# Kernel optimization log

Measured on AMD Instinct MI355X. Metric: run time of the kernel, lower is better.

## Reference

```python
import jax, jax.numpy as jnp
import numpy as np

N_NODES = 50000
N_EDGES = 600000
N_REL = 8
D_IN = 128
D_OUT = 128


def setup_inputs() -> dict:
    key = jax.random.key(0)
    ks = jax.random.split(key, 12)
    s = 1.0 / np.sqrt(D_IN)
    s2 = 1.0 / np.sqrt(2 * D_IN)
    return {
        "x": jax.random.normal(ks[0], (N_NODES, D_IN), jnp.float32),
        "src": jax.random.randint(ks[1], (N_EDGES,), 0, N_NODES, jnp.int32),
        "dst": jax.random.randint(ks[2], (N_EDGES,), 0, N_NODES, jnp.int32),
        "etype": jax.random.randint(ks[3], (N_EDGES,), 0, N_REL, jnp.int32),
        "Wrel": jax.random.normal(ks[4], (N_REL, D_IN, D_OUT), jnp.float32) * s,
        "Wloop": jax.random.normal(ks[5], (D_IN, D_OUT), jnp.float32) * s,
        "brel": jax.random.normal(ks[6], (D_OUT,), jnp.float32) * s,
        "W1": jax.random.normal(ks[7], (2 * D_IN, 2 * D_IN), jnp.float32) * s2,
        "b1": jax.random.normal(ks[8], (2 * D_IN,), jnp.float32) * s2,
        "W2": jax.random.normal(ks[9], (2 * D_IN, D_OUT), jnp.float32) * s2,
        "b2": jax.random.normal(ks[10], (D_OUT,), jnp.float32) * s2,
    }


def rel_graph_conv(x, src, dst, etype, Wrel, Wloop, brel):
    # low_mem style: transform node features once per relation, then gather per edge.
    xW = jnp.einsum('ni,rio->rno', x, Wrel)          # [R, N, D_OUT]
    msg = xW[etype, src]                              # [E, D_OUT] gather by (rel, src)
    agg = jax.ops.segment_sum(msg, dst, num_segments=N_NODES)  # scatter-add to dst
    return agg + x @ Wloop + brel                     # self-loop + bias (DGL defaults)


def reference(x, src, dst, etype, Wrel, Wloop, brel, W1, b1, W2, b2):
    mid = rel_graph_conv(x, src, dst, etype, Wrel, Wloop, brel)
    h = jnp.concatenate([x, mid], axis=1)             # [N, 2*D_IN]
    h = jax.nn.relu(h @ W1 + b1)
    return h @ W2 + b2
```

## Files before the change

### kernel.cpp

```cpp
#include <hip/hip_runtime.h>

#define N_NODES 50000
#define N_EDGES 600000
#define N_REL 8
#define NT_PAD 50176
#define N_TILES 196

typedef __attribute__((ext_vector_type(8))) short bf16x8;
typedef __attribute__((ext_vector_type(4))) float f32x4;

__device__ __forceinline__ ushort f2b(float f) {
    union { float f; unsigned u; } v; v.f = f;
    unsigned r = v.u + 0x7FFFu + ((v.u >> 16) & 1u);
    return (ushort)(r >> 16);
}
__device__ __forceinline__ float b2f(ushort s) {
    union { unsigned u; float f; } v; v.u = ((unsigned)s) << 16;
    return v.f;
}
__device__ __forceinline__ float asf(unsigned u) {
    union { unsigned u; float f; } v; v.u = u;
    return v.f;
}


__global__ void conv_f32_bf16(const float* __restrict__ in, ushort* __restrict__ outb) {
    int i = (blockIdx.x * 256 + threadIdx.x) * 4;
    float4 f = *(const float4*)(in + i);
    ushort4 o; o.x = f2b(f.x); o.y = f2b(f.y); o.z = f2b(f.z); o.w = f2b(f.w);
    *(ushort4*)(outb + i) = o;
}

__global__ void transpose_wts3(const float* __restrict__ Wloop, const float* __restrict__ Wrel,
                               const float* __restrict__ W1, const float* __restrict__ W2,
                               ushort* __restrict__ wt) {
    int y = blockIdx.y;
    if (y == 0) {
        for (int idx = blockIdx.x * 256 + threadIdx.x; idx < 128 * 1152; idx += gridDim.x * 256) {
            int c = idx / 1152, kg = idx - c * 1152;
            float v = (kg < 1024) ? Wrel[(size_t)((kg >> 7) * 128 + (kg & 127)) * 128 + c]
                                  : Wloop[(size_t)(kg - 1024) * 128 + c];
            wt[idx] = f2b(v);
        }
    } else if (y == 1) {
        for (int idx = blockIdx.x * 256 + threadIdx.x; idx < 256 * 256; idx += gridDim.x * 256) {
            int c = idx >> 8, k = idx & 255;
            wt[147456 + idx] = f2b(W1[k * 256 + c]);
        }
    } else {
        for (int idx = blockIdx.x * 256 + threadIdx.x; idx < 128 * 256; idx += gridDim.x * 256) {
            int c = idx >> 8, k = idx & 255;
            wt[212992 + idx] = f2b(W2[k * 128 + c]);
        }
    }
}

template<int NPH, int KMODE, int AS, int CTOT, int OMODE>
__global__ __launch_bounds__(256, 2) void mfma_gemm(
        const ushort* __restrict__ A0, const ushort* __restrict__ A1,
        const ushort* __restrict__ Bt, const float* __restrict__ bias,
        void* __restrict__ outv) {
    __shared__ ushort bs[2][128 * 136];
    const int t = threadIdx.x;
    const int wave = t >> 6, lane = t & 63;
    const int lr = lane & 15, lg = lane >> 4;
    const int wr = (wave >> 1) * 64, wc = (wave & 1) * 64;
    const int row0 = blockIdx.x * 128;
    const ushort* Btb = Bt + (size_t)blockIdx.y * 128 * (NPH * 128);
    const int sgk = (t & 15) * 8;
    const int sc0 = t >> 4;

#define STAGE_LOAD(p)                                                              \
    _Pragma("unroll")                                                              \
    for (int it = 0; it < 8; ++it)                                                 \
        sreg[it] = *(const bf16x8*)(Btb + (size_t)(sc0 + it * 16) * (NPH * 128) +  \
                                    (p) * 128 + sgk);

#define STAGE_WRITE(b)                                                             \
    _Pragma("unroll")                                                              \
    for (int it = 0; it < 8; ++it)                                                 \
        *(bf16x8*)(&bs[b][(sc0 + it * 16) * 136 + sgk]) = sreg[it];

#define LOAD_AF(p, dstf)                                                           \
    {                                                                              \
        const ushort* Ap; int as_;                                                 \
        if (KMODE == 0) {                                                          \
            if ((p) < 8) { Ap = A0 + (p) * 128; as_ = 1024; }                      \
            else         { Ap = A1;             as_ = 128;  }                      \
        } else { Ap = (p) ? A1 : A0; as_ = AS; }                                   \
        _Pragma("unroll")                                                          \
        for (int rt = 0; rt < 4; ++rt) {                                           \
            int ar = row0 + wr + rt * 16 + lr;                                     \
            if (ar >= N_NODES) ar = 0;                                             \
            _Pragma("unroll")                                                      \
            for (int kc = 0; kc < 4; ++kc)                                         \
                dstf[rt][kc] = *(const bf16x8*)(Ap + (size_t)ar * as_ + kc * 32 + lg * 8); \
        }                                                                          \
    }

    f32x4 acc[4][4];
#pragma unroll
    for (int rt = 0; rt < 4; ++rt)
#pragma unroll
        for (int nt = 0; nt < 4; ++nt) acc[rt][nt] = (f32x4){0.f, 0.f, 0.f, 0.f};

    bf16x8 af[4][4], afn[4][4], sreg[8];

    STAGE_LOAD(0);
    LOAD_AF(0, af);
    STAGE_WRITE(0);
    __syncthreads();

#pragma unroll
    for (int p = 0; p < NPH; ++p) {
        if (p + 1 < NPH) {
            STAGE_LOAD(p + 1);
            LOAD_AF(p + 1, afn);
        }
        const ushort* bcur = bs[p & 1];
#pragma unroll
        for (int kc = 0; kc < 4; ++kc) {
            bf16x8 bf[4];
#pragma unroll
            for (int nt = 0; nt < 4; ++nt)
                bf[nt] = *(const bf16x8*)(bcur + (wc + nt * 16 + lr) * 136 + kc * 32 + lg * 8);
#pragma unroll
            for (int rt = 0; rt < 4; ++rt)
#pragma unroll
                for (int nt = 0; nt < 4; ++nt)
                    acc[rt][nt] = __builtin_amdgcn_mfma_f32_16x16x32_bf16(af[rt][kc], bf[nt], acc[rt][nt], 0, 0, 0);
        }
        if (p + 1 < NPH) {
            STAGE_WRITE((p + 1) & 1);
        }
        __syncthreads();
        if (p + 1 < NPH) {
#pragma unroll
            for (int rt = 0; rt < 4; ++rt)
#pragma unroll
                for (int kc = 0; kc < 4; ++kc) af[rt][kc] = afn[rt][kc];
        }
    }

    const int colbase = blockIdx.y * 128;
#pragma unroll
    for (int rt = 0; rt < 4; ++rt) {
#pragma unroll
        for (int nt = 0; nt < 4; ++nt) {
            const int col = colbase + wc + nt * 16 + lr;
            const float bv = bias[col];
#pragma unroll
            for (int j = 0; j < 4; ++j) {
                const int r = row0 + wr + rt * 16 + lg * 4 + j;
                if (r >= N_NODES) continue;
                float vv = acc[rt][nt][j] + bv;
                if (OMODE == 0) {
                    ((float*)outv)[(size_t)r * CTOT + col] = vv;
                } else if (OMODE == 2) {
                    ((ushort*)outv)[(size_t)r * CTOT + col] = f2b(fmaxf(vv, 0.f));
                } else {
                    ((ushort*)outv)[(size_t)r * 128 + col] = f2b(vv);
                }
            }
        }
    }
#undef STAGE_LOAD
#undef STAGE_WRITE
#undef LOAD_AF
}


__global__ void zero_cnt(int* __restrict__ cnt) {
    int i = blockIdx.x * 256 + threadIdx.x;
    if (i < NT_PAD) cnt[i] = 0;
}

__global__ void hist_dst(const int* __restrict__ dst, int* __restrict__ cnt) {
    int e = blockIdx.x * 256 + threadIdx.x;
    if (e < N_EDGES) atomicAdd(&cnt[dst[e]], 1);
}

__global__ void scan_tiles(const int* __restrict__ cnt, int* __restrict__ tincl, int* __restrict__ bsum) {
    __shared__ int s[256];
    int i = blockIdx.x * 256 + threadIdx.x;
    int v = cnt[i];
    s[threadIdx.x] = v;
    __syncthreads();
    for (int off = 1; off < 256; off <<= 1) {
        int add = (threadIdx.x >= off) ? s[threadIdx.x - off] : 0;
        __syncthreads();
        s[threadIdx.x] += add;
        __syncthreads();
    }
    tincl[i] = s[threadIdx.x];
    if (threadIdx.x == 255) bsum[blockIdx.x] = s[255];
}

__global__ void scan_bsum(const int* __restrict__ bsum, int* __restrict__ bex) {
    __shared__ int s[256];
    int v = (threadIdx.x < N_TILES) ? bsum[threadIdx.x] : 0;
    s[threadIdx.x] = v;
    __syncthreads();
    for (int off = 1; off < 256; off <<= 1) {
        int add = (threadIdx.x >= off) ? s[threadIdx.x - off] : 0;
        __syncthreads();
        s[threadIdx.x] += add;
        __syncthreads();
    }
    if (threadIdx.x < N_TILES) bex[threadIdx.x] = s[threadIdx.x] - v;
}

__global__ void finalize_base(const int* __restrict__ cnt, const int* __restrict__ tincl,
                              const int* __restrict__ bex, int* __restrict__ base,
                              int* __restrict__ cursor) {
    int i = blockIdx.x * 256 + threadIdx.x;
    int b = tincl[i] - cnt[i] + bex[blockIdx.x];
    base[i] = b; cursor[i] = b;
}

__global__ void scatter_ids(const int* __restrict__ src, const int* __restrict__ dst,
                            const int* __restrict__ et, int* __restrict__ cursor,
                            unsigned* __restrict__ sorted) {
    int e = blockIdx.x * 256 + threadIdx.x;
    if (e >= N_EDGES) return;
    int pos = atomicAdd(&cursor[dst[e]], 1);
    sorted[pos] = ((unsigned)src[e] << 3) | (unsigned)et[e];
}


#define ACC_ADD(sd, v)                                                       \
    {                                                                        \
        float lo = asf((v) << 16);                                           \
        float hi = asf((v) & 0xffff0000u);                                   \
        switch ((sd) & 7u) {                                                 \
            case 0: a0[0] += lo; a1[0] += hi; asm volatile(""); break;       \
            case 1: a0[1] += lo; a1[1] += hi; asm volatile(""); break;       \
            case 2: a0[2] += lo; a1[2] += hi; asm volatile(""); break;       \
            case 3: a0[3] += lo; a1[3] += hi; asm volatile(""); break;       \
            case 4: a0[4] += lo; a1[4] += hi; asm volatile(""); break;       \
            case 5: a0[5] += lo; a1[5] += hi; asm volatile(""); break;       \
            case 6: a0[6] += lo; a1[6] += hi; asm volatile(""); break;       \
            default: a0[7] += lo; a1[7] += hi; asm volatile(""); break;      \
        }                                                                    \
    }

__global__ __launch_bounds__(256) void gather_agg(
        const unsigned* __restrict__ sorted, const int* __restrict__ base,
        const int* __restrict__ cnt, const ushort* __restrict__ xbf,
        ushort* __restrict__ agg) {
    const int w = threadIdx.x >> 6, lane = threadIdx.x & 63;
    const int n = blockIdx.x * 4 + w;
    const int b = base[n], c = cnt[n];
    const int loff = lane * 2;

    float a0[8], a1[8];
#pragma unroll
    for (int r = 0; r < 8; ++r) { a0[r] = 0.f; a1[r] = 0.f; }

    const unsigned* sp = sorted + b;
    int i = 0;
    for (; i + 4 <= c; i += 4) {
        unsigned s0 = __builtin_amdgcn_readfirstlane(sp[i]);
        unsigned s1 = __builtin_amdgcn_readfirstlane(sp[i + 1]);
        unsigned s2 = __builtin_amdgcn_readfirstlane(sp[i + 2]);
        unsigned s3 = __builtin_amdgcn_readfirstlane(sp[i + 3]);
        unsigned v0 = *(const unsigned*)(xbf + ((size_t)(s0 >> 3) << 7) + loff);
        unsigned v1 = *(const unsigned*)(xbf + ((size_t)(s1 >> 3) << 7) + loff);
        unsigned v2 = *(const unsigned*)(xbf + ((size_t)(s2 >> 3) << 7) + loff);
        unsigned v3 = *(const unsigned*)(xbf + ((size_t)(s3 >> 3) << 7) + loff);
        ACC_ADD(s0, v0); ACC_ADD(s1, v1); ACC_ADD(s2, v2); ACC_ADD(s3, v3);
    }
    for (; i < c; ++i) {
        unsigned sd = __builtin_amdgcn_readfirstlane(sp[i]);
        unsigned v = *(const unsigned*)(xbf + ((size_t)(sd >> 3) << 7) + loff);
        ACC_ADD(sd, v);
    }
#pragma unroll
    for (int r = 0; r < 8; ++r) {
        unsigned pk = (unsigned)f2b(a0[r]) | ((unsigned)f2b(a1[r]) << 16);
        *(unsigned*)(agg + (size_t)n * 1024 + r * 128 + loff) = pk;
    }
}
#undef ACC_ADD


extern "C" void kernel_launch(void* const* d_in, const int* in_sizes, int n_in,
                              void* d_out, int out_size, void* d_ws, size_t ws_size,
                              hipStream_t stream) {
    const float* x     = (const float*)d_in[0];
    const int*   src   = (const int*)  d_in[1];
    const int*   dst   = (const int*)  d_in[2];
    const int*   etype = (const int*)  d_in[3];
    const float* Wrel  = (const float*)d_in[4];
    const float* Wloop = (const float*)d_in[5];
    const float* brel  = (const float*)d_in[6];
    const float* W1    = (const float*)d_in[7];
    const float* b1    = (const float*)d_in[8];
    const float* W2    = (const float*)d_in[9];
    const float* b2    = (const float*)d_in[10];
    float* out = (float*)d_out;

    char* ws = (char*)d_ws;
    ushort* agg   = (ushort*)ws;
    ushort* wt    = (ushort*)(ws + 102400000);
    char* meta    = ws + 102891520;
    int* cnt      = (int*)(meta);
    int* base     = (int*)(meta + 200704);
    int* cursor   = (int*)(meta + 401408);
    int* tincl    = (int*)(meta + 602112);
    int* bsum     = (int*)(meta + 802816);
    int* bex      = (int*)(meta + 803840);
    unsigned* sorted = (unsigned*)(meta + 804864);
    ushort* xbf   = (ushort*)(ws + 106096384);
    ushort* midbf = (ushort*)(ws + 118896384);

    const ushort* wst = wt;
    const ushort* w1t = wt + 147456;
    const ushort* w2t = wt + 212992;
    ushort* h = agg;

    conv_f32_bf16<<<6250, 256, 0, stream>>>(x, xbf);
    transpose_wts3<<<dim3(64, 3), 256, 0, stream>>>(Wloop, Wrel, W1, W2, wt);

    zero_cnt<<<N_TILES, 256, 0, stream>>>(cnt);
    hist_dst<<<(N_EDGES + 255) / 256, 256, 0, stream>>>(dst, cnt);
    scan_tiles<<<N_TILES, 256, 0, stream>>>(cnt, tincl, bsum);
    scan_bsum<<<1, 256, 0, stream>>>(bsum, bex);
    finalize_base<<<N_TILES, 256, 0, stream>>>(cnt, tincl, bex, base, cursor);
    scatter_ids<<<(N_EDGES + 255) / 256, 256, 0, stream>>>(src, dst, etype, cursor, sorted);

    gather_agg<<<N_NODES / 4, 256, 0, stream>>>(sorted, base, cnt, xbf, agg);

    mfma_gemm<9, 0, 0, 128, 4><<<dim3(391, 1), 256, 0, stream>>>(agg, xbf, wst, brel, (void*)midbf);

    mfma_gemm<2, 1, 128, 256, 2><<<dim3(391, 2), 256, 0, stream>>>(xbf, midbf, w1t, b1, (void*)h);

    mfma_gemm<2, 1, 256, 128, 0><<<dim3(391, 1), 256, 0, stream>>>(h, h + 128, w2t, b2, out);
}
```

Measured before the change: 222.7 us.

## Halve GEMM tile rows and K-step to raise occupancy across all three GEMMs

Each MFMA GEMM block now covers 64 rows instead of 128 and steps K in chunks of 64 instead of 128. This halves LDS use and register footprint, allowing launch bounds of 4 blocks per CU and doubling the grid to 782 blocks. The register double-buffering of A fragments is dropped, so A loads are issued synchronously each phase. The change trades prefetch overlap and per-block reuse of the B tile for more waves in flight to hide latency, with more barriers and phases per block.

```diff
diff --git a/kernel.cpp b/kernel.cpp
--- a/kernel.cpp
+++ b/kernel.cpp
@@ -56,95 +56,88 @@
 }
 
 template<int NPH, int KMODE, int AS, int CTOT, int OMODE>
-__global__ __launch_bounds__(256, 2) void mfma_gemm(
+__global__ __launch_bounds__(256, 4) void mfma_gemm(
         const ushort* __restrict__ A0, const ushort* __restrict__ A1,
         const ushort* __restrict__ Bt, const float* __restrict__ bias,
         void* __restrict__ outv) {
-    __shared__ ushort bs[2][128 * 136];
+    __shared__ ushort bs[2][128 * 72];
     const int t = threadIdx.x;
     const int wave = t >> 6, lane = t & 63;
     const int lr = lane & 15, lg = lane >> 4;
-    const int wr = (wave >> 1) * 64, wc = (wave & 1) * 64;
-    const int row0 = blockIdx.x * 128;
-    const ushort* Btb = Bt + (size_t)blockIdx.y * 128 * (NPH * 128);
-    const int sgk = (t & 15) * 8;
-    const int sc0 = t >> 4;
+    const int wr = (wave >> 1) * 32, wc = (wave & 1) * 64;
+    const int row0 = blockIdx.x * 64;
+    const int KTOT = NPH * 64;
+    const ushort* Btb = Bt + (size_t)blockIdx.y * 128 * KTOT;
+    const int sgk = (t & 7) * 8;
+    const int sc0 = t >> 3;
 
 #define STAGE_LOAD(p)                                                              \
     _Pragma("unroll")                                                              \
-    for (int it = 0; it < 8; ++it)                                                 \
-        sreg[it] = *(const bf16x8*)(Btb + (size_t)(sc0 + it * 16) * (NPH * 128) +  \
-                                    (p) * 128 + sgk);
+    for (int it = 0; it < 4; ++it)                                                 \
+        sreg[it] = *(const bf16x8*)(Btb + (size_t)(sc0 + it * 32) * KTOT +         \
+                                    (p) * 64 + sgk);
 
 #define STAGE_WRITE(b)                                                             \
     _Pragma("unroll")                                                              \
-    for (int it = 0; it < 8; ++it)                                                 \
-        *(bf16x8*)(&bs[b][(sc0 + it * 16) * 136 + sgk]) = sreg[it];
-
-#define LOAD_AF(p, dstf)                                                           \
+    for (int it = 0; it < 4; ++it)                                                 \
+        *(bf16x8*)(&bs[b][(sc0 + it * 32) * 72 + sgk]) = sreg[it];
+
+#define LOAD_AF(p)                                                                 \
     {                                                                              \
         const ushort* Ap; int as_;                                                 \
         if (KMODE == 0) {                                                          \
-            if ((p) < 8) { Ap = A0 + (p) * 128; as_ = 1024; }                      \
-            else         { Ap = A1;             as_ = 128;  }                      \
-        } else { Ap = (p) ? A1 : A0; as_ = AS; }                                   \
+            if ((p) < 16) { Ap = A0 + (p) * 64;        as_ = 1024; }               \
+            else          { Ap = A1 + ((p) - 16) * 64; as_ = 128;  }               \
+        } else if (KMODE == 1) {                                                   \
+            if ((p) < NPH / 2) { Ap = A0 + (p) * 64;           as_ = AS; }         \
+            else               { Ap = A1 + ((p) - NPH / 2) * 64; as_ = AS; }       \
+        } else { Ap = A0 + (p) * 64; as_ = AS; }                                   \
         _Pragma("unroll")                                                          \
-        for (int rt = 0; rt < 4; ++rt) {                                           \
+        for (int rt = 0; rt < 2; ++rt) {                                           \
             int ar = row0 + wr + rt * 16 + lr;                                     \
             if (ar >= N_NODES) ar = 0;                                             \
             _Pragma("unroll")                                                      \
-            for (int kc = 0; kc < 4; ++kc)                                         \
-                dstf[rt][kc] = *(const bf16x8*)(Ap + (size_t)ar * as_ + kc * 32 + lg * 8); \
+            for (int kc = 0; kc < 2; ++kc)                                         \
+                af[rt][kc] = *(const bf16x8*)(Ap + (size_t)ar * as_ + kc * 32 + lg * 8); \
         }                                                                          \
     }
 
-    f32x4 acc[4][4];
-#pragma unroll
-    for (int rt = 0; rt < 4; ++rt)
+    f32x4 acc[2][4];
+#pragma unroll
+    for (int rt = 0; rt < 2; ++rt)
 #pragma unroll
         for (int nt = 0; nt < 4; ++nt) acc[rt][nt] = (f32x4){0.f, 0.f, 0.f, 0.f};
 
-    bf16x8 af[4][4], afn[4][4], sreg[8];
+    bf16x8 af[2][2], sreg[4];
 
     STAGE_LOAD(0);
-    LOAD_AF(0, af);
     STAGE_WRITE(0);
     __syncthreads();
 
 #pragma unroll
     for (int p = 0; p < NPH; ++p) {
-        if (p + 1 < NPH) {
-            STAGE_LOAD(p + 1);
-            LOAD_AF(p + 1, afn);
-        }
+        if (p + 1 < NPH) STAGE_LOAD(p + 1);
+        LOAD_AF(p);
         const ushort* bcur = bs[p & 1];
 #pragma unroll
-        for (int kc = 0; kc < 4; ++kc) {
+        for (int kc = 0; kc < 2; ++kc) {
             bf16x8 bf[4];
 #pragma unroll
             for (int nt = 0; nt < 4; ++nt)
-                bf[nt] = *(const bf16x8*)(bcur + (wc + nt * 16 + lr) * 136 + kc * 32 + lg * 8);
-#pragma unroll
-            for (int rt = 0; rt < 4; ++rt)
+                bf[nt] = *(const bf16x8*)(bcur + (wc + nt * 16 + lr) * 72 + kc * 32 + lg * 8);
+#pragma unroll
+            for (int rt = 0; rt < 2; ++rt)
 #pragma unroll
                 for (int nt = 0; nt < 4; ++nt)
                     acc[rt][nt] = __builtin_amdgcn_mfma_f32_16x16x32_bf16(af[rt][kc], bf[nt], acc[rt][nt], 0, 0, 0);
         }
-        if (p + 1 < NPH) {
-            STAGE_WRITE((p + 1) & 1);
-        }
-        __syncthreads();
-        if (p + 1 < NPH) {
-#pragma unroll
-            for (int rt = 0; rt < 4; ++rt)
-#pragma unroll
-                for (int kc = 0; kc < 4; ++kc) af[rt][kc] = afn[rt][kc];
-        }
+        if (p + 1 < NPH) STAGE_WRITE((p + 1) & 1);
+        __syncthreads();
     }
 
     const int colbase = blockIdx.y * 128;
 #pragma unroll
-    for (int rt = 0; rt < 4; ++rt) {
+    for (int rt = 0; rt < 2; ++rt) {
 #pragma unroll
         for (int nt = 0; nt < 4; ++nt) {
             const int col = colbase + wc + nt * 16 + lr;
@@ -331,9 +324,9 @@
 
     gather_agg<<<N_NODES / 4, 256, 0, stream>>>(sorted, base, cnt, xbf, agg);
 
-    mfma_gemm<9, 0, 0, 128, 4><<<dim3(391, 1), 256, 0, stream>>>(agg, xbf, wst, brel, (void*)midbf);
-
-    mfma_gemm<2, 1, 128, 256, 2><<<dim3(391, 2), 256, 0, stream>>>(xbf, midbf, w1t, b1, (void*)h);
-
-    mfma_gemm<2, 1, 256, 128, 0><<<dim3(391, 1), 256, 0, stream>>>(h, h + 128, w2t, b2, out);
-}
+    mfma_gemm<18, 0, 0, 128, 4><<<dim3(782, 1), 256, 0, stream>>>(agg, xbf, wst, brel, (void*)midbf);
+
+    mfma_gemm<4, 1, 128, 256, 2><<<dim3(782, 2), 256, 0, stream>>>(xbf, midbf, w1t, b1, (void*)h);
+
+    mfma_gemm<4, 2, 256, 128, 0><<<dim3(782, 1), 256, 0, stream>>>(h, nullptr, w2t, b2, out);
+}
```

Result: faster. 214.5 us (-3.7%).
